# Performance work log

Measured on AMD Instinct MI355X. Metric: run time of the kernel, lower is better.

The kernel has to match this reference:

```python
import jax, jax.numpy as jnp
import numpy as np

BN_EPS = 1e-5
N_NODES = 100000
N_EDGES = 300000
IN_FEAT = 256
HIDDEN = 128
N_ETYPES = 4


def setup_inputs() -> dict:
    key = jax.random.key(0)
    ks = jax.random.split(key, 10)
    s = 1.0 / np.sqrt(2 * IN_FEAT)
    return {
        "h_src": jax.random.normal(ks[0], (N_NODES, IN_FEAT), jnp.float32),
        "h_dst": jax.random.normal(ks[1], (N_NODES, IN_FEAT), jnp.float32),
        "src_nodes": jax.random.randint(ks[2], (N_EDGES,), 0, N_NODES),
        "dst_nodes": jax.random.randint(ks[3], (N_EDGES,), 0, N_NODES),
        "etype_idx": 0,
        "W1": jax.random.normal(ks[4], (2 * IN_FEAT, HIDDEN), jnp.float32) * s,
        "b1": jnp.zeros((HIDDEN,), jnp.float32),
        "bn_gamma": jnp.ones((HIDDEN,), jnp.float32),
        "bn_beta": jnp.zeros((HIDDEN,), jnp.float32),
        "bn_mean": jnp.zeros((HIDDEN,), jnp.float32),
        "bn_var": jnp.ones((HIDDEN,), jnp.float32),
        "emb": jax.random.normal(ks[5], (N_ETYPES, HIDDEN), jnp.float32),
        "W2": jax.random.normal(ks[6], (HIDDEN, HIDDEN // 2), jnp.float32) * (1.0 / np.sqrt(HIDDEN)),
        "b2": jnp.zeros((HIDDEN // 2,), jnp.float32),
        "W3": jax.random.normal(ks[7], (HIDDEN // 2, 1), jnp.float32) * (1.0 / np.sqrt(HIDDEN // 2)),
        "b3": jnp.zeros((1,), jnp.float32),
    }


def reference(h_src, h_dst, src_nodes, dst_nodes, etype_idx,
              W1, b1, bn_gamma, bn_beta, bn_mean, bn_var,
              emb, W2, b2, W3, b3):
    # gather endpoint features and concat -> [E, 2*in_feat]
    src_feat = h_src[src_nodes]
    dst_feat = h_dst[dst_nodes]
    edge_feat = jnp.concatenate([src_feat, dst_feat], axis=1)
    # Linear + ReLU (Dropout is identity in eval) + BatchNorm1d (running stats)
    x = jax.nn.relu(edge_feat @ W1 + b1)
    x = (x - bn_mean) * jax.lax.rsqrt(bn_var + BN_EPS) * bn_gamma + bn_beta
    # add edge-type embedding (broadcast over edges)
    x = x + emb[etype_idx]
    # per-edge-type predictor MLP -> scalar score per edge
    x = jax.nn.relu(x @ W2 + b2)
    scores = (x @ W3 + b3).squeeze(-1)
    return scores
```

## Files before the change

### kernel.cpp

```cpp
#include <hip/hip_runtime.h>
#include <hip/hip_bf16.h>


typedef __attribute__((ext_vector_type(8))) short bf16x8;
typedef __attribute__((ext_vector_type(4))) float f32x4;
typedef __attribute__((ext_vector_type(8))) unsigned short u16x8;

constexpr int HID   = 128;
constexpr int ETILE = 64;
constexpr int AS    = 72;
constexpr int XS    = 136;
constexpr int PS    = 264;

__device__ inline ushort f2bf(float f) {
    union { __hip_bfloat16 h; ushort u; } cv;
    cv.h = __float2bfloat16(f);
    return cv.u;
}
__device__ inline float bf2f(ushort u) {
    return __uint_as_float(((unsigned int)u) << 16);
}

__global__ __launch_bounds__(256)
void prep_kernel(const float* __restrict__ W1, const float* __restrict__ W2,
                 const float* __restrict__ bn_gamma, const float* __restrict__ bn_beta,
                 const float* __restrict__ bn_mean, const float* __restrict__ bn_var,
                 const float* __restrict__ emb, const int* __restrict__ etype,
                 ushort* __restrict__ B1p, ushort* __restrict__ B2p,
                 float* __restrict__ sc, float* __restrict__ sh)
{
    int i = blockIdx.x * blockDim.x + threadIdx.x;
    if (i < 65536) {
        int j = i & 7, lane = (i >> 3) & 63, ct = (i >> 9) & 7, ks = i >> 12;
        int k = ks * 32 + (lane >> 4) * 8 + j;
        int c = ct * 16 + (lane & 15);
        B1p[i] = f2bf(W1[k * HID + c]);
    } else if (i < 65536 + 8192) {
        int p = i - 65536;
        int j = p & 7, lane = (p >> 3) & 63, ct = (p >> 9) & 3, ks = p >> 11;
        int k = ks * 32 + (lane >> 4) * 8 + j;
        int c = ct * 16 + (lane & 15);
        B2p[p] = f2bf(W2[k * 64 + c]);
    } else if (i < 65536 + 8192 + HID) {
        int c = i - 65536 - 8192;
        float s = bn_gamma[c] * rsqrtf(bn_var[c] + 1e-5f);
        sc[c] = s;
        sh[c] = bn_beta[c] - bn_mean[c] * s + emb[etype[0] * HID + c];
    }
}

__global__ __launch_bounds__(256)
void proj_kernel(const float* __restrict__ h_src, const float* __restrict__ h_dst,
                 const ushort* __restrict__ B1p, const float* __restrict__ b1,
                 ushort* __restrict__ Psrc, ushort* __restrict__ Pdst,
                 int n_nodes, int ntiles, int nblk)
{
    __shared__ ushort sA[ETILE * PS];

    const int t    = threadIdx.x;
    const int lane = t & 63;
    const int w    = t >> 6;
    const int lr   = lane & 15;
    const int lq   = lane >> 4;

#pragma unroll 1
    for (int half = 0; half < 2; ++half) {
        const float* hp = half ? h_dst : h_src;
        ushort* Pp      = half ? Pdst : Psrc;

        bf16x8 bfr[8][2];
#pragma unroll
        for (int ks = 0; ks < 8; ++ks)
#pragma unroll
            for (int ctl = 0; ctl < 2; ++ctl)
                bfr[ks][ctl] = *reinterpret_cast<const bf16x8*>(
                    B1p + (size_t)(((half * 8 + ks) * 8 + 2 * w + ctl) * 64 + lane) * 8);

#pragma unroll 1
        for (int tile = blockIdx.x; tile < ntiles; tile += nblk) {
            const int nb = tile * 64;

            __syncthreads();

#pragma unroll
            for (int i = 0; i < 16; ++i) {
                int f = t + i * 256;
                int e = f >> 6, q = f & 63;
                int row = nb + e;
                if (row >= n_nodes) row = n_nodes - 1;
                float4 v = *reinterpret_cast<const float4*>(
                    hp + (size_t)row * 256 + q * 4);
                ushort4 bv;
                bv.x = f2bf(v.x); bv.y = f2bf(v.y); bv.z = f2bf(v.z); bv.w = f2bf(v.w);
                *reinterpret_cast<ushort4*>(&sA[e * PS + q * 4]) = bv;
            }
            __syncthreads();

            f32x4 acc[4][2];
#pragma unroll
            for (int rt = 0; rt < 4; ++rt)
#pragma unroll
                for (int c = 0; c < 2; ++c) acc[rt][c] = (f32x4)0.0f;

#pragma unroll
            for (int ks = 0; ks < 8; ++ks)
#pragma unroll
                for (int rt = 0; rt < 4; ++rt) {
                    bf16x8 af = *reinterpret_cast<const bf16x8*>(
                        &sA[(rt * 16 + lr) * PS + ks * 32 + lq * 8]);
                    acc[rt][0] = __builtin_amdgcn_mfma_f32_16x16x32_bf16(af, bfr[ks][0], acc[rt][0], 0, 0, 0);
                    acc[rt][1] = __builtin_amdgcn_mfma_f32_16x16x32_bf16(af, bfr[ks][1], acc[rt][1], 0, 0, 0);
                }

            __syncthreads();

#pragma unroll
            for (int ctl = 0; ctl < 2; ++ctl) {
                int c = (2 * w + ctl) * 16 + lr;
                float add = half ? b1[c] : 0.0f;
#pragma unroll
                for (int rt = 0; rt < 4; ++rt)
#pragma unroll
                    for (int r = 0; r < 4; ++r)
                        sA[(rt * 16 + lq * 4 + r) * PS + c] = f2bf(acc[rt][ctl][r] + add);
            }
            __syncthreads();

#pragma unroll
            for (int i = 0; i < 4; ++i) {
                int f = t + i * 256;
                int e = f >> 4, q = f & 15;
                if (nb + e < n_nodes) {
                    u16x8 v = *reinterpret_cast<const u16x8*>(&sA[e * PS + q * 8]);
                    *reinterpret_cast<u16x8*>(Pp + (size_t)(nb + e) * 128 + q * 8) = v;
                }
            }
        }
    }
}

__global__ __launch_bounds__(256)
void edge_kernel(const ushort* __restrict__ Psrc, const ushort* __restrict__ Pdst,
                 const int* __restrict__ src_nodes, const int* __restrict__ dst_nodes,
                 const float* __restrict__ sc, const float* __restrict__ sh,
                 const float* __restrict__ b2, const float* __restrict__ W3,
                 const float* __restrict__ b3, const ushort* __restrict__ B2p,
                 float* __restrict__ out, int n_edges)
{
    __shared__ ushort sX[ETILE * XS];
    __shared__ int s_s[ETILE], s_d[ETILE];

    const int t     = threadIdx.x;
    const int lane  = t & 63;
    const int w     = t >> 6;
    const int lr    = lane & 15;
    const int lq    = lane >> 4;
    const int ebase = blockIdx.x * ETILE;

    if (t < ETILE) {
        int e = ebase + t;
        s_s[t] = src_nodes[e < n_edges ? e : (n_edges - 1)];
    } else if (t < 2 * ETILE) {
        int e = ebase + t - ETILE;
        s_d[t - ETILE] = dst_nodes[e < n_edges ? e : (n_edges - 1)];
    }
    __syncthreads();

    const int eg = w * 16 + lq;
    const int ch = lr;
    u16x8 gs[4], gd[4];
#pragma unroll
    for (int j = 0; j < 4; ++j)
        gs[j] = *reinterpret_cast<const u16x8*>(
            Psrc + (size_t)s_s[eg + j * 4] * 128 + ch * 8);
#pragma unroll
    for (int j = 0; j < 4; ++j)
        gd[j] = *reinterpret_cast<const u16x8*>(
            Pdst + (size_t)s_d[eg + j * 4] * 128 + ch * 8);
    asm volatile("" :: "v"(gs[0]), "v"(gs[1]), "v"(gs[2]), "v"(gs[3]),
                       "v"(gd[0]), "v"(gd[1]), "v"(gd[2]), "v"(gd[3]));

    const int c0 = ch * 8;
    float4 sca = *reinterpret_cast<const float4*>(sc + c0);
    float4 scb = *reinterpret_cast<const float4*>(sc + c0 + 4);
    float4 sha = *reinterpret_cast<const float4*>(sh + c0);
    float4 shb = *reinterpret_cast<const float4*>(sh + c0 + 4);
    float ss[8] = {sca.x, sca.y, sca.z, sca.w, scb.x, scb.y, scb.z, scb.w};
    float zz[8] = {sha.x, sha.y, sha.z, sha.w, shb.x, shb.y, shb.z, shb.w};
#pragma unroll
    for (int j = 0; j < 4; ++j) {
        u16x8 xo;
#pragma unroll
        for (int i = 0; i < 8; ++i) {
            float v = bf2f((ushort)gs[j][i]) + bf2f((ushort)gd[j][i]);
            v = fmaxf(v, 0.0f);
            xo[i] = f2bf(fmaf(v, ss[i], zz[i]));
        }
        *reinterpret_cast<u16x8*>(&sX[(eg + j * 4) * XS + c0]) = xo;
    }
    __syncthreads();

    f32x4 acc2[4];
#pragma unroll
    for (int ct = 0; ct < 4; ++ct) acc2[ct] = (f32x4)0.0f;

#pragma unroll
    for (int ks = 0; ks < 4; ++ks) {
        bf16x8 af = *reinterpret_cast<const bf16x8*>(
            &sX[(w * 16 + lr) * XS + ks * 32 + lq * 8]);
#pragma unroll
        for (int ct = 0; ct < 4; ++ct) {
            bf16x8 bf = *reinterpret_cast<const bf16x8*>(
                B2p + (size_t)((ks * 4 + ct) * 64 + lane) * 8);
            acc2[ct] = __builtin_amdgcn_mfma_f32_16x16x32_bf16(af, bf, acc2[ct], 0, 0, 0);
        }
    }

    float w3v[4], b2v[4];
#pragma unroll
    for (int ct = 0; ct < 4; ++ct) {
        int c = ct * 16 + lr;
        w3v[ct] = W3[c];
        b2v[ct] = b2[c];
    }
#pragma unroll
    for (int r = 0; r < 4; ++r) {
        float sum = 0.0f;
#pragma unroll
        for (int ct = 0; ct < 4; ++ct)
            sum += fmaxf(acc2[ct][r] + b2v[ct], 0.0f) * w3v[ct];
        sum += __shfl_xor(sum, 1);
        sum += __shfl_xor(sum, 2);
        sum += __shfl_xor(sum, 4);
        sum += __shfl_xor(sum, 8);
        int eo = ebase + w * 16 + lq * 4 + r;
        if (lr == 0 && eo < n_edges) out[eo] = sum + b3[0];
    }
}

__global__ __launch_bounds__(256, 3)
void edge_mlp_mfma(const float* __restrict__ h_src, const float* __restrict__ h_dst,
                   const int* __restrict__ src_nodes, const int* __restrict__ dst_nodes,
                   const ushort* __restrict__ B1p, const ushort* __restrict__ B2p,
                   const float* __restrict__ b1, const float* __restrict__ sc,
                   const float* __restrict__ sh, const float* __restrict__ b2,
                   const float* __restrict__ W3, const float* __restrict__ b3,
                   float* __restrict__ out, int n_edges)
{
    __shared__ ushort sA[2][ETILE * AS];
    __shared__ int s_src[ETILE], s_dst[ETILE];

    const int t    = threadIdx.x;
    const int lane = t & 63;
    const int w    = t >> 6;
    const int lr   = lane & 15;
    const int lq   = lane >> 4;
    const int ebase = blockIdx.x * ETILE;

    if (t < ETILE) {
        int e = ebase + t;
        s_src[t] = src_nodes[e < n_edges ? e : 0];
    } else if (t < 2 * ETILE) {
        int e = ebase + t - ETILE;
        s_dst[t - ETILE] = dst_nodes[e < n_edges ? e : 0];
    }

    f32x4 acc[4][2];
#pragma unroll
    for (int rt = 0; rt < 4; ++rt)
#pragma unroll
        for (int c = 0; c < 2; ++c) acc[rt][c] = (f32x4)0.0f;

    float4 rA[4], rB[4];
    bf16x8 Bf0[4], Bf1[4];

#define PHASE_BAR() do {                                                       \
        asm volatile("s_waitcnt lgkmcnt(0)" ::: "memory");                     \
        __builtin_amdgcn_s_barrier();                                          \
    } while (0)
#define PIN() __builtin_amdgcn_sched_barrier(0)

#define LOADC(kc, R) do {                                                      \
        const float* hp = ((kc) < 4) ? h_src : h_dst;                          \
        const int* sidx = ((kc) < 4) ? s_src : s_dst;                          \
        const int koff = ((kc) & 3) * 64;                                      \
        _Pragma("unroll")                                                      \
        for (int i = 0; i < 4; ++i) {                                          \
            int f = t + i * 256; int e = f >> 4; int q = f & 15;               \
            R[i] = *reinterpret_cast<const float4*>(                           \
                hp + (size_t)sidx[e] * 256 + koff + q * 4);                    \
        } } while (0)

#define BLOAD(kc, BR) do {                                                     \
        _Pragma("unroll")                                                      \
        for (int s = 0; s < 2; ++s)                                            \
        _Pragma("unroll")                                                      \
        for (int c = 0; c < 2; ++c)                                            \
            BR[s * 2 + c] = *reinterpret_cast<const bf16x8*>(                  \
                B1p + (size_t)((((kc) * 2 + s) * 8 + 2 * w + c) * 64 + lane) * 8); \
        } while (0)

#define STOREC(B, R) do {                                                      \
        _Pragma("unroll")                                                      \
        for (int i = 0; i < 4; ++i) {                                          \
            int f = t + i * 256; int e = f >> 4; int q = f & 15;               \
            ushort4 bv;                                                        \
            bv.x = f2bf(R[i].x); bv.y = f2bf(R[i].y);                          \
            bv.z = f2bf(R[i].z); bv.w = f2bf(R[i].w);                          \
            *reinterpret_cast<ushort4*>(&sA[B][e * AS + q * 4]) = bv;          \
        } } while (0)

#define COMPF(B, BR) do {                                                      \
        _Pragma("unroll")                                                      \
        for (int ks = 0; ks < 2; ++ks) {                                       \
            _Pragma("unroll")                                                  \
            for (int rt = 0; rt < 4; ++rt) {                                   \
                bf16x8 af = *reinterpret_cast<const bf16x8*>(                  \
                    &sA[B][(rt * 16 + lr) * AS + ks * 32 + lq * 8]);           \
                acc[rt][0] = __builtin_amdgcn_mfma_f32_16x16x32_bf16(af, BR[ks * 2 + 0], acc[rt][0], 0, 0, 0); \
                acc[rt][1] = __builtin_amdgcn_mfma_f32_16x16x32_bf16(af, BR[ks * 2 + 1], acc[rt][1], 0, 0, 0); \
            } } } while (0)

    __syncthreads();

    LOADC(0, rA);
    BLOAD(0, Bf0);
    STOREC(0, rA);
    LOADC(1, rB);
    BLOAD(1, Bf1);
    PHASE_BAR();

    LOADC(2, rA);  PIN();  COMPF(0, Bf0);  BLOAD(2, Bf0);  STOREC(1, rB);  PHASE_BAR();
    LOADC(3, rB);  PIN();  COMPF(1, Bf1);  BLOAD(3, Bf1);  STOREC(0, rA);  PHASE_BAR();
    LOADC(4, rA);  PIN();  COMPF(0, Bf0);  BLOAD(4, Bf0);  STOREC(1, rB);  PHASE_BAR();
    LOADC(5, rB);  PIN();  COMPF(1, Bf1);  BLOAD(5, Bf1);  STOREC(0, rA);  PHASE_BAR();
    LOADC(6, rA);  PIN();  COMPF(0, Bf0);  BLOAD(6, Bf0);  STOREC(1, rB);  PHASE_BAR();
    LOADC(7, rB);  PIN();  COMPF(1, Bf1);  BLOAD(7, Bf1);  STOREC(0, rA);  PHASE_BAR();
                           COMPF(0, Bf0);                  STOREC(1, rB);  PHASE_BAR();
                           COMPF(1, Bf1);

#undef LOADC
#undef BLOAD
#undef STOREC
#undef COMPF
#undef PIN
#undef PHASE_BAR

    __syncthreads();
    ushort* sX = &sA[0][0];
#pragma unroll
    for (int ctl = 0; ctl < 2; ++ctl) {
        int c = (2 * w + ctl) * 16 + lr;
        float bb = b1[c], s = sc[c], z = sh[c];
#pragma unroll
        for (int rt = 0; rt < 4; ++rt)
#pragma unroll
            for (int r = 0; r < 4; ++r) {
                float x = fmaxf(acc[rt][ctl][r] + bb, 0.0f);
                sX[(rt * 16 + lq * 4 + r) * XS + c] = f2bf(fmaf(x, s, z));
            }
    }
    __syncthreads();

    f32x4 acc2[4];
#pragma unroll
    for (int ct = 0; ct < 4; ++ct) acc2[ct] = (f32x4)0.0f;

#pragma unroll
    for (int ks = 0; ks < 4; ++ks) {
        bf16x8 af = *reinterpret_cast<const bf16x8*>(
            &sX[(w * 16 + lr) * XS + ks * 32 + lq * 8]);
#pragma unroll
        for (int ct = 0; ct < 4; ++ct) {
            bf16x8 bf = *reinterpret_cast<const bf16x8*>(
                B2p + (size_t)((ks * 4 + ct) * 64 + lane) * 8);
            acc2[ct] = __builtin_amdgcn_mfma_f32_16x16x32_bf16(af, bf, acc2[ct], 0, 0, 0);
        }
    }

    float w3v[4], b2v[4];
#pragma unroll
    for (int ct = 0; ct < 4; ++ct) {
        int c = ct * 16 + lr;
        w3v[ct] = W3[c];
        b2v[ct] = b2[c];
    }
#pragma unroll
    for (int r = 0; r < 4; ++r) {
        float sum = 0.0f;
#pragma unroll
        for (int ct = 0; ct < 4; ++ct)
            sum += fmaxf(acc2[ct][r] + b2v[ct], 0.0f) * w3v[ct];
        sum += __shfl_xor(sum, 1);
        sum += __shfl_xor(sum, 2);
        sum += __shfl_xor(sum, 4);
        sum += __shfl_xor(sum, 8);
        int e = ebase + w * 16 + lq * 4 + r;
        if (lr == 0 && e < n_edges) out[e] = sum + b3[0];
    }
}

extern "C" void kernel_launch(void* const* d_in, const int* in_sizes, int n_in,
                              void* d_out, int out_size, void* d_ws, size_t ws_size,
                              hipStream_t stream) {
    const float* h_src     = (const float*)d_in[0];
    const float* h_dst     = (const float*)d_in[1];
    const int*   src_nodes = (const int*)d_in[2];
    const int*   dst_nodes = (const int*)d_in[3];
    const int*   etype     = (const int*)d_in[4];
    const float* W1        = (const float*)d_in[5];
    const float* b1        = (const float*)d_in[6];
    const float* bn_gamma  = (const float*)d_in[7];
    const float* bn_beta   = (const float*)d_in[8];
    const float* bn_mean   = (const float*)d_in[9];
    const float* bn_var    = (const float*)d_in[10];
    const float* emb       = (const float*)d_in[11];
    const float* W2        = (const float*)d_in[12];
    const float* b2        = (const float*)d_in[13];
    const float* W3        = (const float*)d_in[14];
    const float* b3        = (const float*)d_in[15];

    const int n_edges = in_sizes[2];
    const int n_nodes = in_sizes[0] / 256;

    ushort* B1p = (ushort*)d_ws;
    ushort* B2p = B1p + 65536;
    float*  scp = (float*)(B2p + 8192);
    float*  shp = scp + HID;
    const size_t wbytes = (size_t)(65536 + 8192) * 2 + 256 * 4;
    const size_t pbytes = (size_t)n_nodes * HID * 2;
    ushort* Psrc = (ushort*)((char*)d_ws + wbytes);
    ushort* Pdst = Psrc + (size_t)n_nodes * HID;

    prep_kernel<<<(65536 + 8192 + HID + 255) / 256, 256, 0, stream>>>(
        W1, W2, bn_gamma, bn_beta, bn_mean, bn_var, emb, etype, B1p, B2p, scp, shp);

    const int egrid = (n_edges + ETILE - 1) / ETILE;

    if (ws_size >= wbytes + 2 * pbytes) {
        const int ntiles = (n_nodes + 63) / 64;
        const int nblk   = (ntiles + 2) / 3;
        proj_kernel<<<nblk, 256, 0, stream>>>(h_src, h_dst, B1p, b1,
                                              Psrc, Pdst, n_nodes, ntiles, nblk);
        edge_kernel<<<egrid, 256, 0, stream>>>(Psrc, Pdst, src_nodes, dst_nodes,
                                               scp, shp, b2, W3, b3, B2p,
                                               (float*)d_out, n_edges);
    } else {
        edge_mlp_mfma<<<egrid, 256, 0, stream>>>(h_src, h_dst, src_nodes, dst_nodes,
                                                 B1p, B2p, b1, scp, shp, b2, W3, b3,
                                                 (float*)d_out, n_edges);
    }
}
```

Baseline: 87.25 us.

## Software-pipeline node projection with double-buffered LDS and register prefetch

The projection kernel now splits each 64-node tile's K dimension into two 128-wide chunks. It prefetches the next chunk into registers while MFMAs run on the current chunk in a ping-pong LDS buffer. Output is written straight from accumulators to global memory instead of being staged through LDS, and the per-tile loop is fully unrolled into a fixed three-tiles-per-block schedule. The edge kernel also hoists the W2 fragments into registers before the gather. The aim is to overlap HBM loads with compute and to cut barriers. In exchange it assumes each block handles at most three tiles and issues narrow 2-byte scattered global stores.

After: 101.7 us. 16.5% more time.

```diff
diff --git a/kernel.cpp b/kernel.cpp
--- a/kernel.cpp
+++ b/kernel.cpp
@@ -10,7 +10,7 @@
 constexpr int ETILE = 64;
 constexpr int AS    = 72;
 constexpr int XS    = 136;
-constexpr int PS    = 264;
+constexpr int CS    = 136;
 
 __device__ inline ushort f2bf(float f) {
     union { __hip_bfloat16 h; ushort u; } cv;
@@ -55,7 +55,7 @@
                  ushort* __restrict__ Psrc, ushort* __restrict__ Pdst,
                  int n_nodes, int ntiles, int nblk)
 {
-    __shared__ ushort sA[ETILE * PS];
+    __shared__ ushort sA[2][ETILE * CS];
 
     const int t    = threadIdx.x;
     const int lane = t & 63;
@@ -63,6 +63,66 @@
     const int lr   = lane & 15;
     const int lq   = lane >> 4;
 
+    float4 rg[8];
+
+#define LOADP(c) do {                                                          \
+        const int tile_ = blockIdx.x + ((c) >> 1) * nblk;                      \
+        const int nb_   = tile_ * 64;                                          \
+        _Pragma("unroll")                                                      \
+        for (int i = 0; i < 8; ++i) {                                          \
+            int f = t + i * 256;                                               \
+            int e = f >> 5, q = f & 31;                                        \
+            int row = nb_ + e;                                                 \
+            if (row >= n_nodes) row = n_nodes - 1;                             \
+            rg[i] = *reinterpret_cast<const float4*>(                          \
+                hp + (size_t)row * 256 + ((c) & 1) * 128 + q * 4);             \
+        } } while (0)
+
+#define STOREP(B) do {                                                         \
+        _Pragma("unroll")                                                      \
+        for (int i = 0; i < 8; ++i) {                                          \
+            int f = t + i * 256;                                               \
+            int e = f >> 5, q = f & 31;                                        \
+            ushort4 bv;                                                        \
+            bv.x = f2bf(rg[i].x); bv.y = f2bf(rg[i].y);                        \
+            bv.z = f2bf(rg[i].z); bv.w = f2bf(rg[i].w);                        \
+            *reinterpret_cast<ushort4*>(&sA[B][e * CS + q * 4]) = bv;          \
+        } } while (0)
+
+#define PCOMP(B, kc) do {                                                      \
+        _Pragma("unroll")                                                      \
+        for (int ks = 0; ks < 4; ++ks)                                         \
+        _Pragma("unroll")                                                      \
+        for (int rt = 0; rt < 4; ++rt) {                                       \
+            bf16x8 af = *reinterpret_cast<const bf16x8*>(                      \
+                &sA[B][(rt * 16 + lr) * CS + ks * 32 + lq * 8]);               \
+            acc[rt][0] = __builtin_amdgcn_mfma_f32_16x16x32_bf16(af, bfr[(kc) * 4 + ks][0], acc[rt][0], 0, 0, 0); \
+            acc[rt][1] = __builtin_amdgcn_mfma_f32_16x16x32_bf16(af, bfr[(kc) * 4 + ks][1], acc[rt][1], 0, 0, 0); \
+        } } while (0)
+
+#define PSTORE(c) do {                                                         \
+        const int tile_ = blockIdx.x + ((c) >> 1) * nblk;                      \
+        const int nb_   = tile_ * 64;                                          \
+        _Pragma("unroll")                                                      \
+        for (int ctl = 0; ctl < 2; ++ctl)                                      \
+        _Pragma("unroll")                                                      \
+        for (int rt = 0; rt < 4; ++rt)                                         \
+        _Pragma("unroll")                                                      \
+        for (int r = 0; r < 4; ++r) {                                          \
+            int row = nb_ + rt * 16 + lq * 4 + r;                              \
+            if (row < n_nodes)                                                 \
+                Pp[(size_t)row * 128 + (2 * w + ctl) * 16 + lr] =              \
+                    f2bf(acc[rt][ctl][r] + b1v[ctl]);                          \
+        } } while (0)
+
+#define ZACC() do {                                                            \
+        _Pragma("unroll")                                                      \
+        for (int rt = 0; rt < 4; ++rt) {                                       \
+            acc[rt][0] = (f32x4)0.0f; acc[rt][1] = (f32x4)0.0f;                \
+        } } while (0)
+
+#define PIN() __builtin_amdgcn_sched_barrier(0)
+
 #pragma unroll 1
     for (int half = 0; half < 2; ++half) {
         const float* hp = half ? h_dst : h_src;
@@ -76,67 +136,32 @@
                 bfr[ks][ctl] = *reinterpret_cast<const bf16x8*>(
                     B1p + (size_t)(((half * 8 + ks) * 8 + 2 * w + ctl) * 64 + lane) * 8);
 
-#pragma unroll 1
-        for (int tile = blockIdx.x; tile < ntiles; tile += nblk) {
-            const int nb = tile * 64;
-
-            __syncthreads();
-
-#pragma unroll
-            for (int i = 0; i < 16; ++i) {
-                int f = t + i * 256;
-                int e = f >> 6, q = f & 63;
-                int row = nb + e;
-                if (row >= n_nodes) row = n_nodes - 1;
-                float4 v = *reinterpret_cast<const float4*>(
-                    hp + (size_t)row * 256 + q * 4);
-                ushort4 bv;
-                bv.x = f2bf(v.x); bv.y = f2bf(v.y); bv.z = f2bf(v.z); bv.w = f2bf(v.w);
-                *reinterpret_cast<ushort4*>(&sA[e * PS + q * 4]) = bv;
-            }
-            __syncthreads();
-
-            f32x4 acc[4][2];
-#pragma unroll
-            for (int rt = 0; rt < 4; ++rt)
-#pragma unroll
-                for (int c = 0; c < 2; ++c) acc[rt][c] = (f32x4)0.0f;
-
-#pragma unroll
-            for (int ks = 0; ks < 8; ++ks)
-#pragma unroll
-                for (int rt = 0; rt < 4; ++rt) {
-                    bf16x8 af = *reinterpret_cast<const bf16x8*>(
-                        &sA[(rt * 16 + lr) * PS + ks * 32 + lq * 8]);
-                    acc[rt][0] = __builtin_amdgcn_mfma_f32_16x16x32_bf16(af, bfr[ks][0], acc[rt][0], 0, 0, 0);
-                    acc[rt][1] = __builtin_amdgcn_mfma_f32_16x16x32_bf16(af, bfr[ks][1], acc[rt][1], 0, 0, 0);
-                }
-
-            __syncthreads();
-
-#pragma unroll
-            for (int ctl = 0; ctl < 2; ++ctl) {
-                int c = (2 * w + ctl) * 16 + lr;
-                float add = half ? b1[c] : 0.0f;
-#pragma unroll
-                for (int rt = 0; rt < 4; ++rt)
-#pragma unroll
-                    for (int r = 0; r < 4; ++r)
-                        sA[(rt * 16 + lq * 4 + r) * PS + c] = f2bf(acc[rt][ctl][r] + add);
-            }
-            __syncthreads();
-
-#pragma unroll
-            for (int i = 0; i < 4; ++i) {
-                int f = t + i * 256;
-                int e = f >> 4, q = f & 15;
-                if (nb + e < n_nodes) {
-                    u16x8 v = *reinterpret_cast<const u16x8*>(&sA[e * PS + q * 8]);
-                    *reinterpret_cast<u16x8*>(Pp + (size_t)(nb + e) * 128 + q * 8) = v;
-                }
-            }
+        float b1v[2] = {0.0f, 0.0f};
+        if (half) {
+            b1v[0] = b1[(2 * w) * 16 + lr];
+            b1v[1] = b1[(2 * w + 1) * 16 + lr];
         }
-    }
+
+        f32x4 acc[4][2];
+
+        __syncthreads();
+        LOADP(0); STOREP(0);
+        __syncthreads();
+
+        LOADP(1);  PIN();  ZACC();  PCOMP(0, 0);                 STOREP(1);  __syncthreads();
+        LOADP(2);  PIN();           PCOMP(1, 1);  PSTORE(1);     STOREP(0);  __syncthreads();
+        LOADP(3);  PIN();  ZACC();  PCOMP(0, 0);                 STOREP(1);  __syncthreads();
+        LOADP(4);  PIN();           PCOMP(1, 1);  PSTORE(3);     STOREP(0);  __syncthreads();
+        LOADP(5);  PIN();  ZACC();  PCOMP(0, 0);                 STOREP(1);  __syncthreads();
+                                    PCOMP(1, 1);  PSTORE(5);
+    }
+
+#undef LOADP
+#undef STOREP
+#undef PCOMP
+#undef PSTORE
+#undef ZACC
+#undef PIN
 }
 
 __global__ __launch_bounds__(256)
@@ -157,6 +182,14 @@
     const int lq    = lane >> 4;
     const int ebase = blockIdx.x * ETILE;
 
+    bf16x8 b2r[4][4];
+#pragma unroll
+    for (int ks = 0; ks < 4; ++ks)
+#pragma unroll
+        for (int ct = 0; ct < 4; ++ct)
+            b2r[ks][ct] = *reinterpret_cast<const bf16x8*>(
+                B2p + (size_t)((ks * 4 + ct) * 64 + lane) * 8);
+
     if (t < ETILE) {
         int e = ebase + t;
         s_s[t] = src_nodes[e < n_edges ? e : (n_edges - 1)];
@@ -209,11 +242,8 @@
         bf16x8 af = *reinterpret_cast<const bf16x8*>(
             &sX[(w * 16 + lr) * XS + ks * 32 + lq * 8]);
 #pragma unroll
-        for (int ct = 0; ct < 4; ++ct) {
-            bf16x8 bf = *reinterpret_cast<const bf16x8*>(
-                B2p + (size_t)((ks * 4 + ct) * 64 + lane) * 8);
-            acc2[ct] = __builtin_amdgcn_mfma_f32_16x16x32_bf16(af, bf, acc2[ct], 0, 0, 0);
-        }
+        for (int ct = 0; ct < 4; ++ct)
+            acc2[ct] = __builtin_amdgcn_mfma_f32_16x16x32_bf16(af, b2r[ks][ct], acc2[ct], 0, 0, 0);
     }
 
     float w3v[4], b2v[4];
```
